# Kernel optimization log

Measured on AMD Instinct MI355X. Metric: run time of the kernel, lower is better.

The kernel has to match this reference:

```python
import jax, jax.numpy as jnp
import numpy as np

B, T, C, NH = 8, 1024, 768, 12
HD = C // NH
NEG = -1e9


def setup_inputs() -> dict:
    key = jax.random.key(0)
    ks = jax.random.split(key, 8)
    s_c = 1.0 / np.sqrt(C)
    s_t = 1.0 / np.sqrt(T)
    return {
        "x": jax.random.normal(ks[0], (B, T, C), dtype=jnp.float32),
        "Wv": jax.random.normal(ks[1], (C, C), dtype=jnp.float32) * s_c,
        "bv": jnp.zeros((C,), dtype=jnp.float32),
        "Wl": jax.random.normal(ks[2], (T, T), dtype=jnp.float32) * s_t,  # weights_layer, no bias
        "Wc": jax.random.normal(ks[3], (T, T), dtype=jnp.float32) * s_t,  # weight_concat
        "bc": jnp.zeros((T,), dtype=jnp.float32),
        "Wp": jax.random.normal(ks[4], (C, C), dtype=jnp.float32) * s_c,
        "bp": jnp.zeros((C,), dtype=jnp.float32),
    }


def reference(x, Wv, bv, Wl, Wc, bc, Wp, bp):
    Bq, Tq, Cq = x.shape
    # NOTE: original forward uses self.value(x) for q, k, and v alike.
    v = x @ Wv.T + bv                              # [B,T,C]
    q = k = v
    # split heads -> [B, nh, T, hd]
    def heads(t):
        return t.reshape(Bq, Tq, NH, HD).transpose(0, 2, 1, 3)
    qh, kh, vh = heads(q), heads(k), heads(v)
    att = jnp.einsum("bhqd,bhkd->bhqk", qh, kh) / jnp.sqrt(jnp.float32(HD))
    # learned seqlen-mixing over the key dim: Linear(T,T) acts on last axis
    att = att @ Wl.T                               # weights_layer (no bias)
    att = att @ Wc.T + bc                          # weight_concat
    # causal mask (tril)
    causal = jnp.tril(jnp.ones((Tq, Tq), dtype=bool))
    att = jnp.where(causal[None, None], att, NEG)
    att = jax.nn.softmax(att, axis=-1)             # attn_drop is identity at eval
    y = jnp.einsum("bhqk,bhkd->bhqd", att, vh)
    y = y.transpose(0, 2, 1, 3).reshape(Bq, Tq, Cq)
    return y @ Wp.T + bp                           # resid_drop identity at eval
```

## Files before the change

### kernel.cpp

```cpp
#include <hip/hip_runtime.h>
#include <stdint.h>

#define Bz 8
#define Tz 1024
#define Cz 768
#define NHz 12
#define HDz 64

typedef unsigned short u16;
typedef __attribute__((ext_vector_type(8))) __bf16 bf16x8;
typedef __attribute__((ext_vector_type(4))) float f32x4;

__device__ __forceinline__ float bf2f(u16 b) {
    union { uint32_t u; float f; } c; c.u = ((uint32_t)b) << 16; return c.f;
}
__device__ __forceinline__ u16 f2bf(float f) {
    union { float f; uint32_t u; } c; c.f = f;
    uint32_t u = c.u;
    return (u16)((u + 0x7fffu + ((u >> 16) & 1u)) >> 16);
}

#define N4_X  (Bz * Tz * Cz / 4)
#define N4_WV (Cz * Cz / 4)
#define N4_WC (Tz * Tz / 4)
#define N4_WP (Cz * Cz / 4)
#define N4_ALL (N4_X + N4_WV + N4_WC + N4_WP)

__global__ __launch_bounds__(256)
void cvt_all(const float* __restrict__ x, const float* __restrict__ wv,
             const float* __restrict__ wc, const float* __restrict__ wp,
             u16* __restrict__ xb, u16* __restrict__ wvb,
             u16* __restrict__ wcb, u16* __restrict__ wpb) {
    int i = blockIdx.x * 256 + threadIdx.x;
    if (i >= N4_ALL) return;
    const float* in;
    u16* out;
    if (i < N4_X) {
        in = x; out = xb;
    } else if (i < N4_X + N4_WV) {
        in = wv; out = wvb; i -= N4_X;
    } else if (i < N4_X + N4_WV + N4_WC) {
        in = wc; out = wcb; i -= N4_X + N4_WV;
    } else {
        in = wp; out = wpb; i -= N4_X + N4_WV + N4_WC;
    }
    float4 v = ((const float4*)in)[i];
    union { u16 h[4]; uint2 u; } o;
    o.h[0] = f2bf(v.x); o.h[1] = f2bf(v.y); o.h[2] = f2bf(v.z); o.h[3] = f2bf(v.w);
    ((uint2*)out)[i] = o.u;
}

template<int BM, int BN, int WM, int WN, bool OUTF32, bool HASBIAS>
__global__ __launch_bounds__(WM * WN * 64)
void gemm_bt(const u16* __restrict__ A, long long sAz, int lda,
             const u16* __restrict__ Bp, long long sBz, int ldb,
             void* __restrict__ Cp, long long sCz, int ldc,
             const float* __restrict__ bias, int K, float alpha) {
    constexpr int NT = WM * WN * 64;
    constexpr int BK = 32;
    constexpr int AI = (BM * BK) / (NT * 8);
    constexpr int BI = (BN * BK) / (NT * 8);
    static_assert(AI >= 1 && (BM * BK) % (NT * 8) == 0, "A staging");
    static_assert(BI >= 1 && (BN * BK) % (NT * 8) == 0, "B staging");
    static_assert(BM == WM * 64 && BN == WN * 64, "wave tiling");

    __shared__ alignas(16) u16 As[2][BM * BK];
    __shared__ alignas(16) u16 Bs[2][BN * BK];

    const int z = blockIdx.z;
    const u16* Ag = A + (long long)z * sAz;
    const u16* Bg = Bp + (long long)z * sBz;

    const int tid = threadIdx.x;
    const int lane = tid & 63;
    const int w = tid >> 6;
    const int wm = w / WN;
    const int wn = w % WN;
    const int rowBase = blockIdx.y * BM;
    const int colBase = blockIdx.x * BN;
    const int koff = (lane >> 4) * 8;
    const int frow = lane & 15;

    auto stage = [&](int buf, int k0) {
#pragma unroll
        for (int i = 0; i < AI; i++) {
            int e = (i * NT + tid) * 8;
            const u16* g = Ag + (long long)(rowBase + (e >> 5)) * lda + k0 + (e & 31);
            __builtin_amdgcn_global_load_lds(
                (const __attribute__((address_space(1))) uint32_t*)g,
                (__attribute__((address_space(3))) uint32_t*)(&As[buf][0] + e), 16, 0, 0);
        }
#pragma unroll
        for (int i = 0; i < BI; i++) {
            int e = (i * NT + tid) * 8;
            const u16* g = Bg + (long long)(colBase + (e >> 5)) * ldb + k0 + (e & 31);
            __builtin_amdgcn_global_load_lds(
                (const __attribute__((address_space(1))) uint32_t*)g,
                (__attribute__((address_space(3))) uint32_t*)(&Bs[buf][0] + e), 16, 0, 0);
        }
    };

    f32x4 acc[4][4] = {};

    const int nk = K / BK;
    stage(0, 0);
    __syncthreads();

#pragma unroll 1
    for (int t = 0; t < nk; ++t) {
        const int cur = t & 1;
        if (t + 1 < nk) stage(cur ^ 1, (t + 1) * BK);

        bf16x8 af[4], bfr[4];
#pragma unroll
        for (int mt = 0; mt < 4; mt++)
            af[mt] = *(const bf16x8*)&As[cur][(wm * 64 + mt * 16 + frow) * BK + koff];
#pragma unroll
        for (int nt = 0; nt < 4; nt++)
            bfr[nt] = *(const bf16x8*)&Bs[cur][(wn * 64 + nt * 16 + frow) * BK + koff];
#pragma unroll
        for (int mt = 0; mt < 4; mt++)
#pragma unroll
            for (int nt = 0; nt < 4; nt++)
                acc[mt][nt] = __builtin_amdgcn_mfma_f32_16x16x32_bf16(
                    af[mt], bfr[nt], acc[mt][nt], 0, 0, 0);

        __syncthreads();
    }

    const int r0 = rowBase + wm * 64;
    const int c0 = colBase + wn * 64;
    const int rl = (lane >> 4) * 4;
    const int cl = lane & 15;
#pragma unroll
    for (int mt = 0; mt < 4; mt++) {
#pragma unroll
        for (int nt = 0; nt < 4; nt++) {
#pragma unroll
            for (int r = 0; r < 4; r++) {
                int row = r0 + mt * 16 + rl + r;
                int col = c0 + nt * 16 + cl;
                float v = acc[mt][nt][r] * alpha;
                if (HASBIAS) v += bias[col];
                if (OUTF32)
                    ((float*)Cp)[(long long)z * sCz + (long long)row * ldc + col] = v;
                else
                    ((u16*)Cp)[(long long)z * sCz + (long long)row * ldc + col] = f2bf(v);
            }
        }
    }
}

template<bool INF32>
__global__ __launch_bounds__(256)
void transpose_to_bf16(const void* __restrict__ in, u16* __restrict__ out,
                       int rows, int cols, long long sInZ, long long sOutZ) {
    __shared__ u16 tile[32][33];
    const int z = blockIdx.z;
    const int c0 = blockIdx.x * 32, r0 = blockIdx.y * 32;
    const int tx = threadIdx.x, ty = threadIdx.y;
#pragma unroll
    for (int i = 0; i < 32; i += 8) {
        long long off = (long long)z * sInZ + (long long)(r0 + ty + i) * cols + c0 + tx;
        tile[ty + i][tx] = INF32 ? f2bf(((const float*)in)[off]) : ((const u16*)in)[off];
    }
    __syncthreads();
#pragma unroll
    for (int i = 0; i < 32; i += 8)
        out[(long long)z * sOutZ + (long long)(c0 + ty + i) * rows + r0 + tx] = tile[tx][ty + i];
}

#define LOG2E 1.44269504f

__global__ __launch_bounds__(512)
void flash_attn(const u16* __restrict__ v, const u16* __restrict__ U,
                const u16* __restrict__ vT, const float* __restrict__ bc,
                u16* __restrict__ y) {
    __shared__ alignas(16) u16 Us[128 * 64];
    __shared__ alignas(16) u16 Vs[64 * 128];
    __shared__ alignas(16) u16 Ps[128 * 136];
    __shared__ u16 bcs[Tz];

    const int bi = blockIdx.x;
    const int xcd = bi & 7;
    const int slot = bi >> 3;
    const int col = (slot % 12) * 8 + xcd;
    const int qi = 7 - slot / 12;
    const int b = col / NHz, h = col % NHz;

    const int tid = threadIdx.x, lane = tid & 63, w = tid >> 6;
    const int quad = lane >> 4, cl = lane & 15;
    const int q0 = qi * 128;
    const int wrow = w * 16;

    for (int j = tid; j < Tz; j += 512) bcs[j] = f2bf(bc[j] * LOG2E);

    const u16* vq = v + ((long long)b * Tz + q0) * Cz + h * HDz;
    bf16x8 aS[2];
#pragma unroll
    for (int ks = 0; ks < 2; ks++)
        aS[ks] = *(const bf16x8*)(vq + (long long)(wrow + cl) * Cz + ks * 32 + quad * 8);

    f32x4 Oacc[4] = {};
    float mrow[4], lrow[4];
#pragma unroll
    for (int r = 0; r < 4; r++) { mrow[r] = -3.0e38f; lrow[r] = 0.f; }

    const u16* Ub = U + (long long)b * Tz * Cz + h * HDz;
    const u16* Vb = vT + ((long long)b * Cz + h * HDz) * Tz;

    __syncthreads();

    const int kts = qi + 1;
    for (int kt = 0; kt < kts; kt++) {
        if (kt) __builtin_amdgcn_s_barrier();
        const u16* Ug = Ub + (long long)kt * 128 * Cz;
#pragma unroll
        for (int i = 0; i < 2; i++) {
            int e = (i * 512 + tid) * 8;
            int key = e >> 6;
            int ch = ((e & 63) >> 3) ^ (key & 7);
            __builtin_amdgcn_global_load_lds(
                (const __attribute__((address_space(1))) uint32_t*)(Ug + (long long)key * Cz + ch * 8),
                (__attribute__((address_space(3))) uint32_t*)(Us + e), 16, 0, 0);
        }
        const u16* Vg = Vb + kt * 128;
#pragma unroll
        for (int i = 0; i < 2; i++) {
            int e = (i * 512 + tid) * 8;
            int dim = e >> 7;
            int ch = ((e & 127) >> 3) ^ (dim & 15);
            __builtin_amdgcn_global_load_lds(
                (const __attribute__((address_space(1))) uint32_t*)(Vg + (long long)dim * Tz + ch * 8),
                (__attribute__((address_space(3))) uint32_t*)(Vs + e), 16, 0, 0);
        }
        asm volatile("s_waitcnt vmcnt(2)" ::: "memory");
        __builtin_amdgcn_s_barrier();

        f32x4 S[8] = {};
        __builtin_amdgcn_s_setprio(1);
#pragma unroll
        for (int ks = 0; ks < 2; ks++)
#pragma unroll
            for (int nt = 0; nt < 8; nt++) {
                int key = nt * 16 + cl;
                bf16x8 bS = *(const bf16x8*)&Us[key * 64 + (((ks * 4 + quad) ^ (key & 7)) * 8)];
                S[nt] = __builtin_amdgcn_mfma_f32_16x16x32_bf16(aS[ks], bS, S[nt], 0, 0, 0);
            }
        __builtin_amdgcn_s_setprio(0);

        const bool last = (kt == kts - 1);
#pragma unroll
        for (int nt = 0; nt < 8; nt++) {
            float bl = bf2f(bcs[kt * 128 + nt * 16 + cl]);
#pragma unroll
            for (int r = 0; r < 4; r++) {
                int rowg = q0 + wrow + quad * 4 + r;
                int colg = kt * 128 + nt * 16 + cl;
                float s = S[nt][r] * (0.125f * LOG2E) + bl;
                if (last && colg > rowg) s = -3.0e38f;
                S[nt][r] = s;
            }
        }

        float mnew[4], alpha[4];
#pragma unroll
        for (int r = 0; r < 4; r++) {
            float m = S[0][r];
#pragma unroll
            for (int nt = 1; nt < 8; nt++) m = fmaxf(m, S[nt][r]);
#pragma unroll
            for (int d = 1; d < 16; d <<= 1) m = fmaxf(m, __shfl_xor(m, d));
            mnew[r] = fmaxf(mrow[r], m);
            alpha[r] = __builtin_amdgcn_exp2f(mrow[r] - mnew[r]);
            mrow[r] = mnew[r];
        }

        float psum[4] = {};
#pragma unroll
        for (int nt = 0; nt < 8; nt++)
#pragma unroll
            for (int r = 0; r < 4; r++) {
                float p = __builtin_amdgcn_exp2f(S[nt][r] - mnew[r]);
                psum[r] += p;
                Ps[(wrow + quad * 4 + r) * 136 + nt * 16 + cl] = f2bf(p);
            }
#pragma unroll
        for (int r = 0; r < 4; r++) {
            float s = psum[r];
#pragma unroll
            for (int d = 1; d < 16; d <<= 1) s += __shfl_xor(s, d);
            lrow[r] = lrow[r] * alpha[r] + s;
#pragma unroll
            for (int nt2 = 0; nt2 < 4; nt2++)
                Oacc[nt2][r] *= alpha[r];
        }

        asm volatile("s_waitcnt vmcnt(0)" ::: "memory");
        __builtin_amdgcn_s_barrier();

        __builtin_amdgcn_s_setprio(1);
#pragma unroll
        for (int ks = 0; ks < 4; ks++) {
            bf16x8 pA = *(const bf16x8*)&Ps[(wrow + cl) * 136 + ks * 32 + quad * 8];
#pragma unroll
            for (int nt2 = 0; nt2 < 4; nt2++) {
                int dim = nt2 * 16 + cl;
                bf16x8 vB = *(const bf16x8*)&Vs[dim * 128 + (((ks * 4 + quad) ^ cl) * 8)];
                Oacc[nt2] = __builtin_amdgcn_mfma_f32_16x16x32_bf16(pA, vB, Oacc[nt2], 0, 0, 0);
            }
        }
        __builtin_amdgcn_s_setprio(0);
    }

    u16* yq = y + ((long long)b * Tz + q0) * Cz + h * HDz;
#pragma unroll
    for (int r = 0; r < 4; r++) {
        float inv = 1.f / lrow[r];
#pragma unroll
        for (int nt2 = 0; nt2 < 4; nt2++)
            yq[(long long)(wrow + quad * 4 + r) * Cz + nt2 * 16 + cl] =
                f2bf(Oacc[nt2][r] * inv);
    }
}

extern "C" void kernel_launch(void* const* d_in, const int* in_sizes, int n_in,
                              void* d_out, int out_size, void* d_ws, size_t ws_size,
                              hipStream_t stream) {
    const float* x  = (const float*)d_in[0];
    const float* Wv = (const float*)d_in[1];
    const float* bv = (const float*)d_in[2];
    const float* Wl = (const float*)d_in[3];
    const float* Wc = (const float*)d_in[4];
    const float* bc = (const float*)d_in[5];
    const float* Wp = (const float*)d_in[6];
    const float* bp = (const float*)d_in[7];

    u16* ws  = (u16*)d_ws;
    u16* xb  = ws;
    u16* Wvb = xb  + (size_t)Bz * Tz * Cz;
    u16* Wcb = Wvb + (size_t)Cz * Cz;
    u16* Wpb = Wcb + (size_t)Tz * Tz;
    u16* WlT = Wpb + (size_t)Cz * Cz;
    u16* Wcl = WlT + (size_t)Tz * Tz;
    u16* vbf = Wcl + (size_t)Tz * Tz;
    u16* vT  = vbf + (size_t)Bz * Tz * Cz;
    u16* U   = vT  + (size_t)Bz * Tz * Cz;

    const long long sTC = (long long)Tz * Cz;
    const long long sCT = (long long)Cz * Tz;

    cvt_all<<<(N4_ALL + 255) / 256, 256, 0, stream>>>(x, Wv, Wc, Wp, xb, Wvb, Wcb, Wpb);
    transpose_to_bf16<true><<<dim3(32, 32, 1), dim3(32, 8), 0, stream>>>(Wl, WlT, Tz, Tz, 0, 0);
    gemm_bt<64, 64, 1, 1, false, false><<<dim3(Tz / 64, Tz / 64, 1), 64, 0, stream>>>(
        Wcb, 0, Tz, WlT, 0, Tz, Wcl, 0, Tz, nullptr, Tz, 1.f);
    gemm_bt<64, 128, 1, 2, false, true><<<dim3(Cz / 128, (Bz * Tz) / 64, 1), 128, 0, stream>>>(
        xb, 0, Cz, Wvb, 0, Cz, vbf, 0, Cz, bv, Cz, 1.f);
    transpose_to_bf16<false><<<dim3(Cz / 32, Tz / 32, Bz), dim3(32, 8), 0, stream>>>(
        vbf, vT, Tz, Cz, sTC, sCT);
    gemm_bt<64, 128, 1, 2, false, false><<<dim3(Cz / 128, Tz / 64, Bz), 128, 0, stream>>>(
        Wcl, 0, Tz, vT, sCT, Tz, U, sTC, Cz, nullptr, Tz, 1.f);
    flash_attn<<<dim3(8 * NHz * Bz, 1, 1), 512, 0, stream>>>(vbf, U, vT, bc, vbf);
    gemm_bt<64, 128, 1, 2, true, true><<<dim3(Cz / 128, (Bz * Tz) / 64, 1), 128, 0, stream>>>(
        vbf, 0, Cz, Wpb, 0, Cz, (float*)d_out, 0, Cz, bp, Cz, 1.f);
}
```

Measured before the change: 235.6 us.

## Prefetch next K/V tiles during attention compute and enlarge GEMM tiles

In the attention kernel, the first U/V tiles are now loaded before the loop. Later U tiles are prefetched into registers during softmax, and the next V tile is issued via global_load_lds after the PV MFMA, so global latency overlaps compute instead of stalling each iteration. The three big GEMMs also move from 64x128 tiles with 128 threads to 128x128 tiles with 256 threads, for more reuse per block at the cost of fewer blocks. The prefetch adds extra barriers and register pressure, and the fewer GEMM blocks may underfill the GPU.

```diff
diff --git a/kernel.cpp b/kernel.cpp
--- a/kernel.cpp
+++ b/kernel.cpp
@@ -10,6 +10,7 @@
 typedef unsigned short u16;
 typedef __attribute__((ext_vector_type(8))) __bf16 bf16x8;
 typedef __attribute__((ext_vector_type(4))) float f32x4;
+typedef __attribute__((ext_vector_type(4))) unsigned int u32x4;
 
 __device__ __forceinline__ float bf2f(u16 b) {
     union { uint32_t u; float f; } c; c.u = ((uint32_t)b) << 16; return c.f;
@@ -209,33 +210,39 @@
     const u16* Ub = U + (long long)b * Tz * Cz + h * HDz;
     const u16* Vb = vT + ((long long)b * Cz + h * HDz) * Tz;
 
+    const int e0 = tid * 8;
+    const int e1 = (512 + tid) * 8;
+    const int ukey0 = e0 >> 6, uch0 = ((e0 & 63) >> 3) ^ (ukey0 & 7);
+    const int ukey1 = e1 >> 6, uch1 = ((e1 & 63) >> 3) ^ (ukey1 & 7);
+    const int vdim0 = e0 >> 7, vch0 = ((e0 & 127) >> 3) ^ (vdim0 & 15);
+    const int vdim1 = e1 >> 7, vch1 = ((e1 & 127) >> 3) ^ (vdim1 & 15);
+
     __syncthreads();
 
     const int kts = qi + 1;
+
+    {
+        const u16* Ug = Ub;
+        __builtin_amdgcn_global_load_lds(
+            (const __attribute__((address_space(1))) uint32_t*)(Ug + (long long)ukey0 * Cz + uch0 * 8),
+            (__attribute__((address_space(3))) uint32_t*)(Us + e0), 16, 0, 0);
+        __builtin_amdgcn_global_load_lds(
+            (const __attribute__((address_space(1))) uint32_t*)(Ug + (long long)ukey1 * Cz + uch1 * 8),
+            (__attribute__((address_space(3))) uint32_t*)(Us + e1), 16, 0, 0);
+        const u16* Vg = Vb;
+        __builtin_amdgcn_global_load_lds(
+            (const __attribute__((address_space(1))) uint32_t*)(Vg + (long long)vdim0 * Tz + vch0 * 8),
+            (__attribute__((address_space(3))) uint32_t*)(Vs + e0), 16, 0, 0);
+        __builtin_amdgcn_global_load_lds(
+            (const __attribute__((address_space(1))) uint32_t*)(Vg + (long long)vdim1 * Tz + vch1 * 8),
+            (__attribute__((address_space(3))) uint32_t*)(Vs + e1), 16, 0, 0);
+        asm volatile("s_waitcnt vmcnt(0)" ::: "memory");
+        __builtin_amdgcn_s_barrier();
+    }
+
+#pragma unroll 1
     for (int kt = 0; kt < kts; kt++) {
-        if (kt) __builtin_amdgcn_s_barrier();
-        const u16* Ug = Ub + (long long)kt * 128 * Cz;
-#pragma unroll
-        for (int i = 0; i < 2; i++) {
-            int e = (i * 512 + tid) * 8;
-            int key = e >> 6;
-            int ch = ((e & 63) >> 3) ^ (key & 7);
-            __builtin_amdgcn_global_load_lds(
-                (const __attribute__((address_space(1))) uint32_t*)(Ug + (long long)key * Cz + ch * 8),
-                (__attribute__((address_space(3))) uint32_t*)(Us + e), 16, 0, 0);
-        }
-        const u16* Vg = Vb + kt * 128;
-#pragma unroll
-        for (int i = 0; i < 2; i++) {
-            int e = (i * 512 + tid) * 8;
-            int dim = e >> 7;
-            int ch = ((e & 127) >> 3) ^ (dim & 15);
-            __builtin_amdgcn_global_load_lds(
-                (const __attribute__((address_space(1))) uint32_t*)(Vg + (long long)dim * Tz + ch * 8),
-                (__attribute__((address_space(3))) uint32_t*)(Vs + e), 16, 0, 0);
-        }
-        asm volatile("s_waitcnt vmcnt(2)" ::: "memory");
-        __builtin_amdgcn_s_barrier();
+        const bool pf = (kt + 1 < kts);
 
         f32x4 S[8] = {};
         __builtin_amdgcn_s_setprio(1);
@@ -248,6 +255,13 @@
                 S[nt] = __builtin_amdgcn_mfma_f32_16x16x32_bf16(aS[ks], bS, S[nt], 0, 0, 0);
             }
         __builtin_amdgcn_s_setprio(0);
+
+        u32x4 u0, u1;
+        if (pf) {
+            const u16* Ug = Ub + (long long)(kt + 1) * 128 * Cz;
+            u0 = *(const u32x4*)(Ug + (long long)ukey0 * Cz + uch0 * 8);
+            u1 = *(const u32x4*)(Ug + (long long)ukey1 * Cz + uch1 * 8);
+        }
 
         const bool last = (kt == kts - 1);
 #pragma unroll
@@ -296,8 +310,11 @@
                 Oacc[nt2][r] *= alpha[r];
         }
 
-        asm volatile("s_waitcnt vmcnt(0)" ::: "memory");
-        __builtin_amdgcn_s_barrier();
+        if (kt) {
+            if (pf) asm volatile("s_waitcnt vmcnt(2)" ::: "memory");
+            else    asm volatile("s_waitcnt vmcnt(0)" ::: "memory");
+            __builtin_amdgcn_s_barrier();
+        }
 
         __builtin_amdgcn_s_setprio(1);
 #pragma unroll
@@ -311,6 +328,22 @@
             }
         }
         __builtin_amdgcn_s_setprio(0);
+
+        if (pf) {
+            __builtin_amdgcn_s_barrier();
+            asm volatile("s_waitcnt vmcnt(0)" ::: "memory");
+            *(u32x4*)(Us + e0) = u0;
+            *(u32x4*)(Us + e1) = u1;
+            const u16* Vg = Vb + (kt + 1) * 128;
+            __builtin_amdgcn_global_load_lds(
+                (const __attribute__((address_space(1))) uint32_t*)(Vg + (long long)vdim0 * Tz + vch0 * 8),
+                (__attribute__((address_space(3))) uint32_t*)(Vs + e0), 16, 0, 0);
+            __builtin_amdgcn_global_load_lds(
+                (const __attribute__((address_space(1))) uint32_t*)(Vg + (long long)vdim1 * Tz + vch1 * 8),
+                (__attribute__((address_space(3))) uint32_t*)(Vs + e1), 16, 0, 0);
+            asm volatile("s_waitcnt lgkmcnt(0)" ::: "memory");
+            __builtin_amdgcn_s_barrier();
+        }
     }
 
     u16* yq = y + ((long long)b * Tz + q0) * Cz + h * HDz;
@@ -354,13 +387,13 @@
     transpose_to_bf16<true><<<dim3(32, 32, 1), dim3(32, 8), 0, stream>>>(Wl, WlT, Tz, Tz, 0, 0);
     gemm_bt<64, 64, 1, 1, false, false><<<dim3(Tz / 64, Tz / 64, 1), 64, 0, stream>>>(
         Wcb, 0, Tz, WlT, 0, Tz, Wcl, 0, Tz, nullptr, Tz, 1.f);
-    gemm_bt<64, 128, 1, 2, false, true><<<dim3(Cz / 128, (Bz * Tz) / 64, 1), 128, 0, stream>>>(
+    gemm_bt<128, 128, 2, 2, false, true><<<dim3(Cz / 128, (Bz * Tz) / 128, 1), 256, 0, stream>>>(
         xb, 0, Cz, Wvb, 0, Cz, vbf, 0, Cz, bv, Cz, 1.f);
     transpose_to_bf16<false><<<dim3(Cz / 32, Tz / 32, Bz), dim3(32, 8), 0, stream>>>(
         vbf, vT, Tz, Cz, sTC, sCT);
-    gemm_bt<64, 128, 1, 2, false, false><<<dim3(Cz / 128, Tz / 64, Bz), 128, 0, stream>>>(
+    gemm_bt<128, 128, 2, 2, false, false><<<dim3(Cz / 128, Tz / 128, Bz), 256, 0, stream>>>(
         Wcl, 0, Tz, vT, sCT, Tz, U, sTC, Cz, nullptr, Tz, 1.f);
     flash_attn<<<dim3(8 * NHz * Bz, 1, 1), 512, 0, stream>>>(vbf, U, vT, bc, vbf);
-    gemm_bt<64, 128, 1, 2, true, true><<<dim3(Cz / 128, (Bz * Tz) / 64, 1), 128, 0, stream>>>(
+    gemm_bt<128, 128, 2, 2, true, true><<<dim3(Cz / 128, (Bz * Tz) / 128, 1), 256, 0, stream>>>(
         vbf, 0, Cz, Wpb, 0, Cz, (float*)d_out, 0, Cz, bp, Cz, 1.f);
 }
```

Measured after the change: 234.2 us. Within noise of the previous version (-0.6%).
